# Kernel tuning notes

Hardware: AMD Instinct MI355X
Metric: run time of the kernel (lower is better)

## Reference

```python
import jax, jax.numpy as jnp
import numpy as np

HIDDEN = 4096
N_EXPERTS = 128
TOP_K = 8
N_GROUP = 1
TOPK_GROUP = 1
ROUTED_SCALING = 1.0
NORM_TOPK_PROB = True


def setup_inputs() -> dict:
    key = jax.random.key(0)
    k1, k2 = jax.random.split(key)
    tokens = 16384  # batch 4 * seq 4096
    hidden_states = jax.random.normal(k1, (tokens, HIDDEN), dtype=jnp.float32)
    # router gate weight (n_routed_experts, hidden_size)
    weight = jax.random.normal(k2, (N_EXPERTS, HIDDEN), dtype=jnp.float32) * 0.02
    # e_score_correction_bias buffer, initialized to zeros in the module
    e_score_correction_bias = jnp.zeros((N_EXPERTS,), dtype=jnp.float32)
    return {"hidden_states": hidden_states, "weight": weight,
            "e_score_correction_bias": e_score_correction_bias}


def _get_topk_indices(scores, bias):
    # scores: [T, E] sigmoid gate scores; bias: [E]
    T = scores.shape[0]
    experts_per_group = N_EXPERTS // N_GROUP
    s = scores + bias[None, :]  # scores_for_choice
    # group score: sum of top-2 corrected scores within each group
    grp = s.reshape(T, N_GROUP, experts_per_group)
    group_scores = jnp.sum(jax.lax.top_k(grp, 2)[0], axis=-1)  # [T, G]
    group_idx = jax.lax.top_k(group_scores, TOPK_GROUP)[1]      # [T, topk_group]
    group_mask = jnp.zeros((T, N_GROUP), dtype=bool).at[
        jnp.arange(T)[:, None], group_idx].set(True)
    score_mask = jnp.repeat(group_mask, experts_per_group, axis=-1)  # [T, E]
    s_masked = jnp.where(score_mask, s, 0.0)
    topk_indices = jax.lax.top_k(s_masked, TOP_K)[1]  # [T, top_k]
    return topk_indices


def reference(hidden_states, weight, e_score_correction_bias):
    x = hidden_states.reshape(-1, HIDDEN).astype(jnp.float32)
    router_logits = x @ weight.astype(jnp.float32).T          # [T, E]
    scores = jax.nn.sigmoid(router_logits)
    topk_indices = _get_topk_indices(scores, e_score_correction_bias)
    topk_weights = jnp.take_along_axis(scores, topk_indices, axis=1)  # [T, top_k]
    if NORM_TOPK_PROB:
        denom = jnp.sum(topk_weights, axis=-1, keepdims=True) + 1e-20
        topk_weights = topk_weights / denom
    topk_weights = topk_weights * ROUTED_SCALING
    return topk_indices, topk_weights
```

## Files before the change

### kernel.cpp

```cpp
#include <hip/hip_runtime.h>
#include <math.h>

#define HIDDEN 4096
#define NEXP   128
#define TOPK   8
#define BT     32
#define CHUNK  64
#define NCHUNK (HIDDEN / CHUNK)
#define SSTR   132
#define PLANE  (NEXP * CHUNK)

typedef int v4i __attribute__((ext_vector_type(4)));

static __device__ __forceinline__ unsigned pack4(int a, int b, int c, int d) {
    return (unsigned)(a & 255) | ((unsigned)(b & 255) << 8) |
           ((unsigned)(c & 255) << 16) | ((unsigned)(d & 255) << 24);
}

static __device__ __forceinline__ void slice5(float val, float scale1,
        int& d0, int& d1, int& d2, int& d3, int& d4) {
    float v = val * scale1;
    float f = __builtin_rintf(v);
    float r = v - f;
    int nh = (int)f;
    int nl = (int)__builtin_rintf(r * 2097152.0f);
    d0 = (nh + 64) >> 7;  d1 = nh - (d0 << 7);
    d2 = (nl + 8192) >> 14;
    int r2 = nl - (d2 << 14);
    d3 = (r2 + 64) >> 7;  d4 = r2 - (d3 << 7);
}

static __device__ __forceinline__ void slice4(float val, float scale1,
        int& d0, int& d1, int& d2, int& d3) {
    float v = val * scale1;
    float f = __builtin_rintf(v);
    float r = v - f;
    int nh = (int)f;
    int nl = (int)__builtin_rintf(r * 16384.0f);
    d0 = (nh + 64) >> 7;  d1 = nh - (d0 << 7);
    d2 = (nl + 64) >> 7;  d3 = nl - (d2 << 7);
}

__global__ __launch_bounds__(256)
void slice_w_kernel(const float* __restrict__ W, signed char* __restrict__ P)
{
    const int t  = blockIdx.x * 256 + threadIdx.x;
    const int e  = t >> 9;
    const int k0 = (t & 511) * 8;
    const float* src = W + (size_t)e * HIDDEN + k0;
    const float4 a = ((const float4*)src)[0];
    const float4 b = ((const float4*)src)[1];

    int p00,p01,p02,p03,p04; slice5(a.x, 32768.0f, p00,p01,p02,p03,p04);
    int p10,p11,p12,p13,p14; slice5(a.y, 32768.0f, p10,p11,p12,p13,p14);
    int p20,p21,p22,p23,p24; slice5(a.z, 32768.0f, p20,p21,p22,p23,p24);
    int p30,p31,p32,p33,p34; slice5(a.w, 32768.0f, p30,p31,p32,p33,p34);
    int p40,p41,p42,p43,p44; slice5(b.x, 32768.0f, p40,p41,p42,p43,p44);
    int p50,p51,p52,p53,p54; slice5(b.y, 32768.0f, p50,p51,p52,p53,p54);
    int p60,p61,p62,p63,p64; slice5(b.z, 32768.0f, p60,p61,p62,p63,p64);
    int p70,p71,p72,p73,p74; slice5(b.w, 32768.0f, p70,p71,p72,p73,p74);

    const int c = k0 >> 6, kin = k0 & 63;
    signed char* base = P + ((size_t)(c * 5) * NEXP + e) * CHUNK + kin;
    uint2 v;
    v.x = pack4(p00,p10,p20,p30); v.y = pack4(p40,p50,p60,p70);
    *(uint2*)(base + 0 * PLANE) = v;
    v.x = pack4(p01,p11,p21,p31); v.y = pack4(p41,p51,p61,p71);
    *(uint2*)(base + 1 * PLANE) = v;
    v.x = pack4(p02,p12,p22,p32); v.y = pack4(p42,p52,p62,p72);
    *(uint2*)(base + 2 * PLANE) = v;
    v.x = pack4(p03,p13,p23,p33); v.y = pack4(p43,p53,p63,p73);
    *(uint2*)(base + 3 * PLANE) = v;
    v.x = pack4(p04,p14,p24,p34); v.y = pack4(p44,p54,p64,p74);
    *(uint2*)(base + 4 * PLANE) = v;
}

static __device__ __forceinline__ void slice_store_x(char* dst, float4 xa, float4 xb)
{
    int a00,a01,a02,a03; slice4(xa.x, 1024.0f, a00,a01,a02,a03);
    int a10,a11,a12,a13; slice4(xa.y, 1024.0f, a10,a11,a12,a13);
    int a20,a21,a22,a23; slice4(xa.z, 1024.0f, a20,a21,a22,a23);
    int a30,a31,a32,a33; slice4(xa.w, 1024.0f, a30,a31,a32,a33);
    int a40,a41,a42,a43; slice4(xb.x, 1024.0f, a40,a41,a42,a43);
    int a50,a51,a52,a53; slice4(xb.y, 1024.0f, a50,a51,a52,a53);
    int a60,a61,a62,a63; slice4(xb.z, 1024.0f, a60,a61,a62,a63);
    int a70,a71,a72,a73; slice4(xb.w, 1024.0f, a70,a71,a72,a73);
    uint2 v;
    v.x = pack4(a00,a10,a20,a30); v.y = pack4(a40,a50,a60,a70);
    *(uint2*)(dst + 0 * 2048) = v;
    v.x = pack4(a01,a11,a21,a31); v.y = pack4(a41,a51,a61,a71);
    *(uint2*)(dst + 1 * 2048) = v;
    v.x = pack4(a02,a12,a22,a32); v.y = pack4(a42,a52,a62,a72);
    *(uint2*)(dst + 2 * 2048) = v;
    v.x = pack4(a03,a13,a23,a33); v.y = pack4(a43,a53,a63,a73);
    *(uint2*)(dst + 3 * 2048) = v;
}

#define MFMA_BLOCK(BF, BUF)                                                    \
    {                                                                          \
        _Pragma("unroll")                                                      \
        for (int tt = 0; tt < 2; tt++) {                                       \
            const char* ap = Ast + (BUF) + (tt ? rph1 : rph0);                 \
            const v4i a0 = *(const v4i*)(ap + 0 * 2048);                       \
            const v4i a1 = *(const v4i*)(ap + 1 * 2048);                       \
            const v4i a2 = *(const v4i*)(ap + 2 * 2048);                       \
            const v4i a3 = *(const v4i*)(ap + 3 * 2048);                       \
            _Pragma("unroll")                                                  \
            for (int et = 0; et < 2; et++) {                                   \
                acc[tt][et][0] = __builtin_amdgcn_mfma_i32_16x16x64_i8(a0, BF[et][0], acc[tt][et][0], 0, 0, 0); \
                acc[tt][et][1] = __builtin_amdgcn_mfma_i32_16x16x64_i8(a0, BF[et][1], acc[tt][et][1], 0, 0, 0); \
                acc[tt][et][1] = __builtin_amdgcn_mfma_i32_16x16x64_i8(a1, BF[et][0], acc[tt][et][1], 0, 0, 0); \
                acc[tt][et][2] = __builtin_amdgcn_mfma_i32_16x16x64_i8(a0, BF[et][2], acc[tt][et][2], 0, 0, 0); \
                acc[tt][et][2] = __builtin_amdgcn_mfma_i32_16x16x64_i8(a1, BF[et][1], acc[tt][et][2], 0, 0, 0); \
                acc[tt][et][2] = __builtin_amdgcn_mfma_i32_16x16x64_i8(a2, BF[et][0], acc[tt][et][2], 0, 0, 0); \
                acc[tt][et][3] = __builtin_amdgcn_mfma_i32_16x16x64_i8(a0, BF[et][3], acc[tt][et][3], 0, 0, 0); \
                acc[tt][et][3] = __builtin_amdgcn_mfma_i32_16x16x64_i8(a1, BF[et][2], acc[tt][et][3], 0, 0, 0); \
                acc[tt][et][3] = __builtin_amdgcn_mfma_i32_16x16x64_i8(a2, BF[et][1], acc[tt][et][3], 0, 0, 0); \
                acc[tt][et][3] = __builtin_amdgcn_mfma_i32_16x16x64_i8(a3, BF[et][0], acc[tt][et][3], 0, 0, 0); \
                acc[tt][et][4] = __builtin_amdgcn_mfma_i32_16x16x64_i8(a0, BF[et][4], acc[tt][et][4], 0, 0, 0); \
                acc[tt][et][4] = __builtin_amdgcn_mfma_i32_16x16x64_i8(a1, BF[et][3], acc[tt][et][4], 0, 0, 0); \
                acc[tt][et][4] = __builtin_amdgcn_mfma_i32_16x16x64_i8(a2, BF[et][2], acc[tt][et][4], 0, 0, 0); \
                acc[tt][et][4] = __builtin_amdgcn_mfma_i32_16x16x64_i8(a3, BF[et][1], acc[tt][et][4], 0, 0, 0); \
            }                                                                  \
        }                                                                      \
    }

__global__ __launch_bounds__(256, 2)
void router_kernel(const float* __restrict__ X,
                   const signed char* __restrict__ P,
                   const float* __restrict__ Bias,
                   float* __restrict__ Out, int T)
{
    __shared__ double S[BT * SSTR];
    char* Ast = (char*)S;

    const int tid  = threadIdx.x;
    const int lane = tid & 63;
    const int wave = tid >> 6;
    const int tokBase = blockIdx.x * BT;

    const int sm  = tid & 31;
    const int sk8 = tid >> 5;
    int srow = tokBase + sm; if (srow >= T) srow = T - 1;
    const float* xptr = X + (size_t)srow * HIDDEN + sk8 * 8;
    const int su    = sm * 4 + (sk8 >> 1);
    const int swoff = ((su ^ ((su >> 3) & 7)) << 4) + (sk8 & 1) * 8;

    const int ru0  = ((lane & 15)     ) * 4 + (lane >> 4);
    const int ru1  = ((lane & 15) + 16) * 4 + (lane >> 4);
    const int rph0 = (ru0 ^ ((ru0 >> 3) & 7)) << 4;
    const int rph1 = (ru1 ^ ((ru1 >> 3) & 7)) << 4;

    const int eb0 = wave * 32 + (lane & 15);
    const int koff = (lane >> 4) * 16;
    const size_t boff0 = (size_t)eb0 * CHUNK + koff;
    const size_t boff1 = boff0 + (size_t)16 * CHUNK;

    v4i acc[2][2][5];
    #pragma unroll
    for (int tt = 0; tt < 2; tt++)
        #pragma unroll
        for (int et = 0; et < 2; et++)
            #pragma unroll
            for (int s = 0; s < 5; s++)
                acc[tt][et][s] = (v4i){0,0,0,0};

    float4 xa = ((const float4*)xptr)[0];
    float4 xb = ((const float4*)xptr)[1];
    slice_store_x(Ast + swoff, xa, xb);

    v4i bfA[2][5], bfB[2][5];
    #pragma unroll
    for (int s = 0; s < 5; s++) {
        bfA[0][s] = *(const v4i*)(P + (size_t)s * PLANE + boff0);
        bfA[1][s] = *(const v4i*)(P + (size_t)s * PLANE + boff1);
    }
    __syncthreads();

    #pragma unroll 1
    for (int c = 0; c < NCHUNK; c += 2) {
        {
            const signed char* pn = P + (size_t)((c + 1) * 5) * PLANE;
            #pragma unroll
            for (int s = 0; s < 5; s++) {
                bfB[0][s] = *(const v4i*)(pn + (size_t)s * PLANE + boff0);
                bfB[1][s] = *(const v4i*)(pn + (size_t)s * PLANE + boff1);
            }
            const float* nx = xptr + (c + 1) * CHUNK;
            xa = ((const float4*)nx)[0];
            xb = ((const float4*)nx)[1];

            MFMA_BLOCK(bfA, 0)

            slice_store_x(Ast + 8192 + swoff, xa, xb);
            __syncthreads();
        }
        {
            if (c + 2 < NCHUNK) {
                const signed char* pn = P + (size_t)((c + 2) * 5) * PLANE;
                #pragma unroll
                for (int s = 0; s < 5; s++) {
                    bfA[0][s] = *(const v4i*)(pn + (size_t)s * PLANE + boff0);
                    bfA[1][s] = *(const v4i*)(pn + (size_t)s * PLANE + boff1);
                }
                const float* nx = xptr + (c + 2) * CHUNK;
                xa = ((const float4*)nx)[0];
                xb = ((const float4*)nx)[1];
            }

            MFMA_BLOCK(bfB, 8192)

            if (c + 2 < NCHUNK) {
                slice_store_x(Ast + swoff, xa, xb);
            }
            __syncthreads();
        }
    }

    {
        const double w0 = 0x1p-11, w1 = 0x1p-18, w2 = 0x1p-25, w3 = 0x1p-32, w4 = 0x1p-39;
        #pragma unroll
        for (int tt = 0; tt < 2; tt++)
            #pragma unroll
            for (int et = 0; et < 2; et++) {
                const int ecol = wave * 32 + et * 16 + (lane & 15);
                const double bias = (double)Bias[ecol];
                #pragma unroll
                for (int r = 0; r < 4; r++) {
                    const int trow = tt * 16 + (lane >> 4) * 4 + r;
                    const double logit = (double)acc[tt][et][0][r] * w0
                                       + (double)acc[tt][et][1][r] * w1
                                       + (double)acc[tt][et][2][r] * w2
                                       + (double)acc[tt][et][3][r] * w3
                                       + (double)acc[tt][et][4][r] * w4;
                    S[trow * SSTR + ecol] = 1.0 / (1.0 + exp(-logit)) + bias;
                }
            }
    }
    __syncthreads();

    {
        const int tk  = tid >> 3;
        const int j   = tid & 7;
        const int tok = tokBase + tk;
        const double* row = S + tk * SSTR + j * 16;
        double v[16];
        #pragma unroll
        for (int k = 0; k < 16; k++) v[k] = row[k];

        double wts[TOPK]; float idxf[TOPK];
        double wsum = 0.0;
        #pragma unroll
        for (int p = 0; p < TOPK; p++) {
            double best = v[0]; int bi = 0;
            #pragma unroll
            for (int k = 1; k < 16; k++)
                if (v[k] > best) { best = v[k]; bi = k; }
            int be = j * 16 + bi;
            #pragma unroll
            for (int off = 1; off < 8; off <<= 1) {
                double ob = __shfl_xor(best, off, 8);
                int    oe = __shfl_xor(be,   off, 8);
                if (ob > best || (ob == best && oe < be)) { best = ob; be = oe; }
            }
            const bool own = (be >> 4) == j;
            const int  bl  = be & 15;
            #pragma unroll
            for (int k = 0; k < 16; k++)
                if (own && k == bl) v[k] = -1.0e300;
            const double sg = best - (double)Bias[be];
            wts[p]  = sg;
            wsum   += sg;
            idxf[p] = (float)be;
        }
        if (j == 0 && tok < T) {
            const double inv = 1.0 / (wsum + 1e-20);
            float* oi = Out + (size_t)tok * TOPK;
            float* ow = Out + (size_t)T * TOPK + (size_t)tok * TOPK;
            #pragma unroll
            for (int p = 0; p < TOPK; p++) {
                oi[p] = idxf[p];
                ow[p] = (float)(wts[p] * inv);
            }
        }
    }
}

extern "C" void kernel_launch(void* const* d_in, const int* in_sizes, int n_in,
                              void* d_out, int out_size, void* d_ws, size_t ws_size,
                              hipStream_t stream) {
    const float* X    = (const float*)d_in[0];
    const float* W    = (const float*)d_in[1];
    const float* Bias = (const float*)d_in[2];
    float* Out = (float*)d_out;
    const int T = in_sizes[0] / HIDDEN;
    signed char* P = (signed char*)d_ws;

    hipLaunchKernelGGL(slice_w_kernel, dim3(NEXP * 512 / 256), dim3(256), 0, stream, W, P);
    hipLaunchKernelGGL(router_kernel, dim3((T + BT - 1) / BT), dim3(256), 0, stream,
                       X, P, Bias, Out, T);
}
```

Before: 449.2 us.

## Halve token tile to 16 and raise occupancy with simpler per-chunk loop

Cuts the token tile per block from 32 to 16, which halves the accumulator registers and allows launch bounds of 4 blocks per CU instead of 2. The manual double-buffered register prefetch of B slices is replaced by a simple per-chunk loop that loads B directly before the MFMAs, relying on more resident waves to hide latency. In exchange, each block reuses every B load for half as many tokens, so global/L2 traffic for the sliced weights doubles and per-block sync overhead rises relative to compute.

```diff
diff --git a/kernel.cpp b/kernel.cpp
--- a/kernel.cpp
+++ b/kernel.cpp
@@ -4,7 +4,7 @@
 #define HIDDEN 4096
 #define NEXP   128
 #define TOPK   8
-#define BT     32
+#define BT     16
 #define CHUNK  64
 #define NCHUNK (HIDDEN / CHUNK)
 #define SSTR   132
@@ -75,57 +75,19 @@
     *(uint2*)(base + 4 * PLANE) = v;
 }
 
-static __device__ __forceinline__ void slice_store_x(char* dst, float4 xa, float4 xb)
+static __device__ __forceinline__ void slice_store_x4(char* dst, float4 xa)
 {
     int a00,a01,a02,a03; slice4(xa.x, 1024.0f, a00,a01,a02,a03);
     int a10,a11,a12,a13; slice4(xa.y, 1024.0f, a10,a11,a12,a13);
     int a20,a21,a22,a23; slice4(xa.z, 1024.0f, a20,a21,a22,a23);
     int a30,a31,a32,a33; slice4(xa.w, 1024.0f, a30,a31,a32,a33);
-    int a40,a41,a42,a43; slice4(xb.x, 1024.0f, a40,a41,a42,a43);
-    int a50,a51,a52,a53; slice4(xb.y, 1024.0f, a50,a51,a52,a53);
-    int a60,a61,a62,a63; slice4(xb.z, 1024.0f, a60,a61,a62,a63);
-    int a70,a71,a72,a73; slice4(xb.w, 1024.0f, a70,a71,a72,a73);
-    uint2 v;
-    v.x = pack4(a00,a10,a20,a30); v.y = pack4(a40,a50,a60,a70);
-    *(uint2*)(dst + 0 * 2048) = v;
-    v.x = pack4(a01,a11,a21,a31); v.y = pack4(a41,a51,a61,a71);
-    *(uint2*)(dst + 1 * 2048) = v;
-    v.x = pack4(a02,a12,a22,a32); v.y = pack4(a42,a52,a62,a72);
-    *(uint2*)(dst + 2 * 2048) = v;
-    v.x = pack4(a03,a13,a23,a33); v.y = pack4(a43,a53,a63,a73);
-    *(uint2*)(dst + 3 * 2048) = v;
-}
-
-#define MFMA_BLOCK(BF, BUF)                                                    \
-    {                                                                          \
-        _Pragma("unroll")                                                      \
-        for (int tt = 0; tt < 2; tt++) {                                       \
-            const char* ap = Ast + (BUF) + (tt ? rph1 : rph0);                 \
-            const v4i a0 = *(const v4i*)(ap + 0 * 2048);                       \
-            const v4i a1 = *(const v4i*)(ap + 1 * 2048);                       \
-            const v4i a2 = *(const v4i*)(ap + 2 * 2048);                       \
-            const v4i a3 = *(const v4i*)(ap + 3 * 2048);                       \
-            _Pragma("unroll")                                                  \
-            for (int et = 0; et < 2; et++) {                                   \
-                acc[tt][et][0] = __builtin_amdgcn_mfma_i32_16x16x64_i8(a0, BF[et][0], acc[tt][et][0], 0, 0, 0); \
-                acc[tt][et][1] = __builtin_amdgcn_mfma_i32_16x16x64_i8(a0, BF[et][1], acc[tt][et][1], 0, 0, 0); \
-                acc[tt][et][1] = __builtin_amdgcn_mfma_i32_16x16x64_i8(a1, BF[et][0], acc[tt][et][1], 0, 0, 0); \
-                acc[tt][et][2] = __builtin_amdgcn_mfma_i32_16x16x64_i8(a0, BF[et][2], acc[tt][et][2], 0, 0, 0); \
-                acc[tt][et][2] = __builtin_amdgcn_mfma_i32_16x16x64_i8(a1, BF[et][1], acc[tt][et][2], 0, 0, 0); \
-                acc[tt][et][2] = __builtin_amdgcn_mfma_i32_16x16x64_i8(a2, BF[et][0], acc[tt][et][2], 0, 0, 0); \
-                acc[tt][et][3] = __builtin_amdgcn_mfma_i32_16x16x64_i8(a0, BF[et][3], acc[tt][et][3], 0, 0, 0); \
-                acc[tt][et][3] = __builtin_amdgcn_mfma_i32_16x16x64_i8(a1, BF[et][2], acc[tt][et][3], 0, 0, 0); \
-                acc[tt][et][3] = __builtin_amdgcn_mfma_i32_16x16x64_i8(a2, BF[et][1], acc[tt][et][3], 0, 0, 0); \
-                acc[tt][et][3] = __builtin_amdgcn_mfma_i32_16x16x64_i8(a3, BF[et][0], acc[tt][et][3], 0, 0, 0); \
-                acc[tt][et][4] = __builtin_amdgcn_mfma_i32_16x16x64_i8(a0, BF[et][4], acc[tt][et][4], 0, 0, 0); \
-                acc[tt][et][4] = __builtin_amdgcn_mfma_i32_16x16x64_i8(a1, BF[et][3], acc[tt][et][4], 0, 0, 0); \
-                acc[tt][et][4] = __builtin_amdgcn_mfma_i32_16x16x64_i8(a2, BF[et][2], acc[tt][et][4], 0, 0, 0); \
-                acc[tt][et][4] = __builtin_amdgcn_mfma_i32_16x16x64_i8(a3, BF[et][1], acc[tt][et][4], 0, 0, 0); \
-            }                                                                  \
-        }                                                                      \
-    }
-
-__global__ __launch_bounds__(256, 2)
+    *(unsigned*)(dst + 0 * 1024) = pack4(a00, a10, a20, a30);
+    *(unsigned*)(dst + 1 * 1024) = pack4(a01, a11, a21, a31);
+    *(unsigned*)(dst + 2 * 1024) = pack4(a02, a12, a22, a32);
+    *(unsigned*)(dst + 3 * 1024) = pack4(a03, a13, a23, a33);
+}
+
+__global__ __launch_bounds__(256, 4)
 void router_kernel(const float* __restrict__ X,
                    const signed char* __restrict__ P,
                    const float* __restrict__ Bias,
@@ -139,107 +101,95 @@
     const int wave = tid >> 6;
     const int tokBase = blockIdx.x * BT;
 
-    const int sm  = tid & 31;
-    const int sk8 = tid >> 5;
+    const int sm  = tid & 15;
+    const int sk4 = tid >> 4;
     int srow = tokBase + sm; if (srow >= T) srow = T - 1;
-    const float* xptr = X + (size_t)srow * HIDDEN + sk8 * 8;
-    const int su    = sm * 4 + (sk8 >> 1);
-    const int swoff = ((su ^ ((su >> 3) & 7)) << 4) + (sk8 & 1) * 8;
-
-    const int ru0  = ((lane & 15)     ) * 4 + (lane >> 4);
-    const int ru1  = ((lane & 15) + 16) * 4 + (lane >> 4);
+    const float* xptr = X + (size_t)srow * HIDDEN + sk4 * 4;
+    const int su    = sm * 4 + (sk4 >> 2);
+    const int swoff = ((su ^ ((su >> 3) & 7)) << 4) + (sk4 & 3) * 4;
+
+    const int ru0  = (lane & 15) * 4 + (lane >> 4);
     const int rph0 = (ru0 ^ ((ru0 >> 3) & 7)) << 4;
-    const int rph1 = (ru1 ^ ((ru1 >> 3) & 7)) << 4;
 
     const int eb0 = wave * 32 + (lane & 15);
     const int koff = (lane >> 4) * 16;
     const size_t boff0 = (size_t)eb0 * CHUNK + koff;
     const size_t boff1 = boff0 + (size_t)16 * CHUNK;
 
-    v4i acc[2][2][5];
+    v4i acc[2][5];
     #pragma unroll
-    for (int tt = 0; tt < 2; tt++)
-        #pragma unroll
-        for (int et = 0; et < 2; et++)
-            #pragma unroll
-            for (int s = 0; s < 5; s++)
-                acc[tt][et][s] = (v4i){0,0,0,0};
-
-    float4 xa = ((const float4*)xptr)[0];
-    float4 xb = ((const float4*)xptr)[1];
-    slice_store_x(Ast + swoff, xa, xb);
-
-    v4i bfA[2][5], bfB[2][5];
-    #pragma unroll
-    for (int s = 0; s < 5; s++) {
-        bfA[0][s] = *(const v4i*)(P + (size_t)s * PLANE + boff0);
-        bfA[1][s] = *(const v4i*)(P + (size_t)s * PLANE + boff1);
+    for (int et = 0; et < 2; et++)
+        #pragma unroll
+        for (int s = 0; s < 5; s++)
+            acc[et][s] = (v4i){0, 0, 0, 0};
+
+    float4 xa = *(const float4*)xptr;
+    slice_store_x4(Ast + swoff, xa);
+    __syncthreads();
+
+    #pragma unroll 2
+    for (int c = 0; c < NCHUNK; c++) {
+        const int buf = (c & 1) * 4096;
+        if (c + 1 < NCHUNK)
+            xa = *(const float4*)(xptr + (c + 1) * CHUNK);
+
+        const char* ap = Ast + buf + rph0;
+        const v4i a0 = *(const v4i*)(ap + 0 * 1024);
+        const v4i a1 = *(const v4i*)(ap + 1 * 1024);
+        const v4i a2 = *(const v4i*)(ap + 2 * 1024);
+        const v4i a3 = *(const v4i*)(ap + 3 * 1024);
+
+        const signed char* pc = P + (size_t)(c * 5) * PLANE;
+        #pragma unroll
+        for (int et = 0; et < 2; et++) {
+            const size_t bo = et ? boff1 : boff0;
+            const v4i b0 = *(const v4i*)(pc + (size_t)0 * PLANE + bo);
+            const v4i b1 = *(const v4i*)(pc + (size_t)1 * PLANE + bo);
+            const v4i b2 = *(const v4i*)(pc + (size_t)2 * PLANE + bo);
+            const v4i b3 = *(const v4i*)(pc + (size_t)3 * PLANE + bo);
+            const v4i b4 = *(const v4i*)(pc + (size_t)4 * PLANE + bo);
+            acc[et][0] = __builtin_amdgcn_mfma_i32_16x16x64_i8(a0, b0, acc[et][0], 0, 0, 0);
+            acc[et][1] = __builtin_amdgcn_mfma_i32_16x16x64_i8(a0, b1, acc[et][1], 0, 0, 0);
+            acc[et][1] = __builtin_amdgcn_mfma_i32_16x16x64_i8(a1, b0, acc[et][1], 0, 0, 0);
+            acc[et][2] = __builtin_amdgcn_mfma_i32_16x16x64_i8(a0, b2, acc[et][2], 0, 0, 0);
+            acc[et][2] = __builtin_amdgcn_mfma_i32_16x16x64_i8(a1, b1, acc[et][2], 0, 0, 0);
+            acc[et][2] = __builtin_amdgcn_mfma_i32_16x16x64_i8(a2, b0, acc[et][2], 0, 0, 0);
+            acc[et][3] = __builtin_amdgcn_mfma_i32_16x16x64_i8(a0, b3, acc[et][3], 0, 0, 0);
+            acc[et][3] = __builtin_amdgcn_mfma_i32_16x16x64_i8(a1, b2, acc[et][3], 0, 0, 0);
+            acc[et][3] = __builtin_amdgcn_mfma_i32_16x16x64_i8(a2, b1, acc[et][3], 0, 0, 0);
+            acc[et][3] = __builtin_amdgcn_mfma_i32_16x16x64_i8(a3, b0, acc[et][3], 0, 0, 0);
+            acc[et][4] = __builtin_amdgcn_mfma_i32_16x16x64_i8(a0, b4, acc[et][4], 0, 0, 0);
+            acc[et][4] = __builtin_amdgcn_mfma_i32_16x16x64_i8(a1, b3, acc[et][4], 0, 0, 0);
+            acc[et][4] = __builtin_amdgcn_mfma_i32_16x16x64_i8(a2, b2, acc[et][4], 0, 0, 0);
+            acc[et][4] = __builtin_amdgcn_mfma_i32_16x16x64_i8(a3, b1, acc[et][4], 0, 0, 0);
+        }
+
+        if (c + 1 < NCHUNK)
+            slice_store_x4(Ast + (buf ^ 4096) + swoff, xa);
+        __syncthreads();
+    }
+
+    {
+        const double w0 = 0x1p-11, w1 = 0x1p-18, w2 = 0x1p-25, w3 = 0x1p-32, w4 = 0x1p-39;
+        #pragma unroll
+        for (int et = 0; et < 2; et++) {
+            const int ecol = wave * 32 + et * 16 + (lane & 15);
+            const double bias = (double)Bias[ecol];
+            #pragma unroll
+            for (int r = 0; r < 4; r++) {
+                const int trow = (lane >> 4) * 4 + r;
+                const double logit = (double)acc[et][0][r] * w0
+                                   + (double)acc[et][1][r] * w1
+                                   + (double)acc[et][2][r] * w2
+                                   + (double)acc[et][3][r] * w3
+                                   + (double)acc[et][4][r] * w4;
+                S[trow * SSTR + ecol] = 1.0 / (1.0 + exp(-logit)) + bias;
+            }
+        }
     }
     __syncthreads();
 
-    #pragma unroll 1
-    for (int c = 0; c < NCHUNK; c += 2) {
-        {
-            const signed char* pn = P + (size_t)((c + 1) * 5) * PLANE;
-            #pragma unroll
-            for (int s = 0; s < 5; s++) {
-                bfB[0][s] = *(const v4i*)(pn + (size_t)s * PLANE + boff0);
-                bfB[1][s] = *(const v4i*)(pn + (size_t)s * PLANE + boff1);
-            }
-            const float* nx = xptr + (c + 1) * CHUNK;
-            xa = ((const float4*)nx)[0];
-            xb = ((const float4*)nx)[1];
-
-            MFMA_BLOCK(bfA, 0)
-
-            slice_store_x(Ast + 8192 + swoff, xa, xb);
-            __syncthreads();
-        }
-        {
-            if (c + 2 < NCHUNK) {
-                const signed char* pn = P + (size_t)((c + 2) * 5) * PLANE;
-                #pragma unroll
-                for (int s = 0; s < 5; s++) {
-                    bfA[0][s] = *(const v4i*)(pn + (size_t)s * PLANE + boff0);
-                    bfA[1][s] = *(const v4i*)(pn + (size_t)s * PLANE + boff1);
-                }
-                const float* nx = xptr + (c + 2) * CHUNK;
-                xa = ((const float4*)nx)[0];
-                xb = ((const float4*)nx)[1];
-            }
-
-            MFMA_BLOCK(bfB, 8192)
-
-            if (c + 2 < NCHUNK) {
-                slice_store_x(Ast + swoff, xa, xb);
-            }
-            __syncthreads();
-        }
-    }
-
-    {
-        const double w0 = 0x1p-11, w1 = 0x1p-18, w2 = 0x1p-25, w3 = 0x1p-32, w4 = 0x1p-39;
-        #pragma unroll
-        for (int tt = 0; tt < 2; tt++)
-            #pragma unroll
-            for (int et = 0; et < 2; et++) {
-                const int ecol = wave * 32 + et * 16 + (lane & 15);
-                const double bias = (double)Bias[ecol];
-                #pragma unroll
-                for (int r = 0; r < 4; r++) {
-                    const int trow = tt * 16 + (lane >> 4) * 4 + r;
-                    const double logit = (double)acc[tt][et][0][r] * w0
-                                       + (double)acc[tt][et][1][r] * w1
-                                       + (double)acc[tt][et][2][r] * w2
-                                       + (double)acc[tt][et][3][r] * w3
-                                       + (double)acc[tt][et][4][r] * w4;
-                    S[trow * SSTR + ecol] = 1.0 / (1.0 + exp(-logit)) + bias;
-                }
-            }
-    }
-    __syncthreads();
-
-    {
+    if (tid < BT * 8) {
         const int tk  = tid >> 3;
         const int j   = tid & 7;
         const int tok = tokBase + tk;
```

Result: slower. 513.3 us (+14.3%).

## Drop lowest-order MFMA slice term and deepen X prefetch with lighter barriers

Applied to the files above, without the earlier changes.

Removes the a0*B4 cross-term from the sliced int8 GEMM, so each block issues 13 MFMAs per tile instead of 14. The fifth weight slice is no longer loaded, which cuts register use and global traffic for weight fragments. X loads are now prefetched one chunk further ahead, with wrap-around addressing so no branches are needed. __syncthreads is replaced by an LDS-only waitcnt plus s_barrier. Dropping the lowest-order term adds small precision error to the logits, which could change near-tie top-k selections.

```diff
diff --git a/kernel.cpp b/kernel.cpp
--- a/kernel.cpp
+++ b/kernel.cpp
@@ -96,7 +96,7 @@
     *(uint2*)(dst + 3 * 2048) = v;
 }
 
-#define MFMA_BLOCK(BF, BUF)                                                    \
+#define MFMA13(BF, BUF)                                                        \
     {                                                                          \
         _Pragma("unroll")                                                      \
         for (int tt = 0; tt < 2; tt++) {                                       \
@@ -117,7 +117,6 @@
                 acc[tt][et][3] = __builtin_amdgcn_mfma_i32_16x16x64_i8(a1, BF[et][2], acc[tt][et][3], 0, 0, 0); \
                 acc[tt][et][3] = __builtin_amdgcn_mfma_i32_16x16x64_i8(a2, BF[et][1], acc[tt][et][3], 0, 0, 0); \
                 acc[tt][et][3] = __builtin_amdgcn_mfma_i32_16x16x64_i8(a3, BF[et][0], acc[tt][et][3], 0, 0, 0); \
-                acc[tt][et][4] = __builtin_amdgcn_mfma_i32_16x16x64_i8(a0, BF[et][4], acc[tt][et][4], 0, 0, 0); \
                 acc[tt][et][4] = __builtin_amdgcn_mfma_i32_16x16x64_i8(a1, BF[et][3], acc[tt][et][4], 0, 0, 0); \
                 acc[tt][et][4] = __builtin_amdgcn_mfma_i32_16x16x64_i8(a2, BF[et][2], acc[tt][et][4], 0, 0, 0); \
                 acc[tt][et][4] = __builtin_amdgcn_mfma_i32_16x16x64_i8(a3, BF[et][1], acc[tt][et][4], 0, 0, 0); \
@@ -163,57 +162,62 @@
         for (int et = 0; et < 2; et++)
             #pragma unroll
             for (int s = 0; s < 5; s++)
-                acc[tt][et][s] = (v4i){0,0,0,0};
-
-    float4 xa = ((const float4*)xptr)[0];
-    float4 xb = ((const float4*)xptr)[1];
-    slice_store_x(Ast + swoff, xa, xb);
-
-    v4i bfA[2][5], bfB[2][5];
+                acc[tt][et][s] = (v4i){0, 0, 0, 0};
+
+    {
+        float4 xa = ((const float4*)xptr)[0];
+        float4 xb = ((const float4*)xptr)[1];
+        slice_store_x(Ast + swoff, xa, xb);
+    }
+    v4i bfE[2][4], bfO[2][4];
     #pragma unroll
-    for (int s = 0; s < 5; s++) {
-        bfA[0][s] = *(const v4i*)(P + (size_t)s * PLANE + boff0);
-        bfA[1][s] = *(const v4i*)(P + (size_t)s * PLANE + boff1);
-    }
-    __syncthreads();
-
+    for (int s = 0; s < 4; s++) {
+        bfE[0][s] = *(const v4i*)(P + (size_t)s * PLANE + boff0);
+        bfE[1][s] = *(const v4i*)(P + (size_t)s * PLANE + boff1);
+    }
+    float4 xoa = ((const float4*)(xptr + CHUNK))[0];
+    float4 xob = ((const float4*)(xptr + CHUNK))[1];
+
+    asm volatile("s_waitcnt lgkmcnt(0)" ::: "memory");
+    __builtin_amdgcn_s_barrier();
+
+    float4 xea, xeb;
     #pragma unroll 1
     for (int c = 0; c < NCHUNK; c += 2) {
         {
             const signed char* pn = P + (size_t)((c + 1) * 5) * PLANE;
             #pragma unroll
-            for (int s = 0; s < 5; s++) {
-                bfB[0][s] = *(const v4i*)(pn + (size_t)s * PLANE + boff0);
-                bfB[1][s] = *(const v4i*)(pn + (size_t)s * PLANE + boff1);
-            }
-            const float* nx = xptr + (c + 1) * CHUNK;
-            xa = ((const float4*)nx)[0];
-            xb = ((const float4*)nx)[1];
-
-            MFMA_BLOCK(bfA, 0)
-
-            slice_store_x(Ast + 8192 + swoff, xa, xb);
-            __syncthreads();
+            for (int s = 0; s < 4; s++) {
+                bfO[0][s] = *(const v4i*)(pn + (size_t)s * PLANE + boff0);
+                bfO[1][s] = *(const v4i*)(pn + (size_t)s * PLANE + boff1);
+            }
+            const float* nx = xptr + ((c + 2) & (NCHUNK - 1)) * CHUNK;
+            xea = ((const float4*)nx)[0];
+            xeb = ((const float4*)nx)[1];
+
+            MFMA13(bfE, 0)
+
+            slice_store_x(Ast + 8192 + swoff, xoa, xob);
+            asm volatile("s_waitcnt lgkmcnt(0)" ::: "memory");
+            __builtin_amdgcn_s_barrier();
         }
         {
-            if (c + 2 < NCHUNK) {
-                const signed char* pn = P + (size_t)((c + 2) * 5) * PLANE;
-                #pragma unroll
-                for (int s = 0; s < 5; s++) {
-                    bfA[0][s] = *(const v4i*)(pn + (size_t)s * PLANE + boff0);
-                    bfA[1][s] = *(const v4i*)(pn + (size_t)s * PLANE + boff1);
-                }
-                const float* nx = xptr + (c + 2) * CHUNK;
-                xa = ((const float4*)nx)[0];
-                xb = ((const float4*)nx)[1];
-            }
-
-            MFMA_BLOCK(bfB, 8192)
-
-            if (c + 2 < NCHUNK) {
-                slice_store_x(Ast + swoff, xa, xb);
-            }
-            __syncthreads();
+            const signed char* pn = P + (size_t)(((c + 2) & (NCHUNK - 1)) * 5) * PLANE;
+            #pragma unroll
+            for (int s = 0; s < 4; s++) {
+                bfE[0][s] = *(const v4i*)(pn + (size_t)s * PLANE + boff0);
+                bfE[1][s] = *(const v4i*)(pn + (size_t)s * PLANE + boff1);
+            }
+            const float* nx = xptr + ((c + 3) & (NCHUNK - 1)) * CHUNK;
+            xoa = ((const float4*)nx)[0];
+            xob = ((const float4*)nx)[1];
+
+            MFMA13(bfO, 8192)
+
+            if (c + 2 < NCHUNK)
+                slice_store_x(Ast + swoff, xea, xeb);
+            asm volatile("s_waitcnt lgkmcnt(0)" ::: "memory");
+            __builtin_amdgcn_s_barrier();
         }
     }
 
```

Result: faster. 417.9 us (-7.0%).
